# Kernel tuning notes

Measured on AMD Instinct MI355X. Metric: run time of the kernel, lower is better.

Reference implementation:

```python
import jax, jax.numpy as jnp
import numpy as np


def setup_inputs() -> dict:
    key = jax.random.key(0)
    k1, k2, k3 = jax.random.split(key, 3)
    B, T, D = 64, 256, 512
    real = jax.random.normal(k1, (B, T, D), dtype=jnp.float32)
    imag = jax.random.normal(k2, (B, T, D), dtype=jnp.float32)
    weight = jax.random.uniform(k3, (B, T, 1), dtype=jnp.float32)
    return {"real": real, "imag": imag, "weight": weight}


def reference(real, imag, weight):
    # Weighted complex outer-product mixture:
    #   out_r[b] = sum_t w[b,t] * (r_t r_t^T + i_t i_t^T)
    #   out_i[b] = sum_t w[b,t] * (i_t r_t^T - r_t i_t^T)
    # Equivalent to the original per-sample loop + TxDxD outer products,
    # but fused: scale one operand by w and contract over t directly.
    w = weight[..., 0]  # [B, T]
    rw = real * w[..., None]  # [B, T, D]
    iw = imag * w[..., None]
    out_r = jnp.einsum('btd,bte->bde', rw, real) + jnp.einsum('btd,bte->bde', iw, imag)
    out_i = jnp.einsum('btd,bte->bde', iw, real) - jnp.einsum('btd,bte->bde', rw, imag)
    return (out_r, out_i)
```

## Files before the change

kernel.cpp:

```cpp
#include <hip/hip_runtime.h>
#include <cstdint>
#include <cstddef>

#define BB 64
#define TT 256
#define DD 512
#define BK 32
#define TILEM 128

typedef short bf16x8 __attribute__((ext_vector_type(8)));
typedef float f32x4  __attribute__((ext_vector_type(4)));
typedef int   i32x4  __attribute__((ext_vector_type(4)));

static __device__ __forceinline__ unsigned short f2bf(float x) {
  unsigned u = __builtin_bit_cast(unsigned, x) + 0x8000u;
  return (unsigned short)(u >> 16);
}

__global__ __launch_bounds__(256, 2)
void ComplexMixture_54838142435828_kernel(const float* __restrict__ re,
                                          const float* __restrict__ im,
                                          const float* __restrict__ wt,
                                          float* __restrict__ out) {
  __shared__ __attribute__((aligned(16))) unsigned short sAr[4 * 128 * 8];
  __shared__ __attribute__((aligned(16))) unsigned short sAi[4 * 128 * 8];
  __shared__ __attribute__((aligned(16))) unsigned short sBr[4 * 128 * 8];
  __shared__ __attribute__((aligned(16))) unsigned short sBi[4 * 128 * 8];
  __shared__ float sw[TT];

  const int tid = threadIdx.x;

  const int L = blockIdx.x;
  const int c = L & 7;
  const int s = L >> 3;
  const int b  = c * 8 + (s >> 4);
  const int t5 = s & 15;
  const int d0 = (t5 >> 2) * TILEM;
  const int e0 = (t5 & 3) * TILEM;

  sw[tid] = wt[b * TT + tid];

  const int lane = tid & 63;
  const int wid  = tid >> 6;
  const int wm = (wid >> 1) * 64;
  const int wn = (wid & 1) * 64;
  const int quad = lane >> 4;
  const int l16  = lane & 15;

  f32x4 accR[4][4], accI[4][4];
  #pragma unroll
  for (int mt = 0; mt < 4; ++mt)
    #pragma unroll
    for (int nt = 0; nt < 4; ++nt) {
      accR[mt][nt] = (f32x4){0.f, 0.f, 0.f, 0.f};
      accI[mt][nt] = (f32x4){0.f, 0.f, 0.f, 0.f};
    }

  const int sd = tid & 127;
  const int kh = tid >> 7;

  for (int kt = 0; kt < TT; kt += BK) {
    __syncthreads();

    const int kb = kt + kh * 16;
    const size_t rowBase = ((size_t)(b * TT + kb)) * DD;

    {
      const float* pr = re + rowBase + d0 + sd;
      const float* pi = im + rowBase + d0 + sd;
      #pragma unroll
      for (int cc = 0; cc < 2; ++cc) {
        union { unsigned short h[8]; i32x4 q; } ur, ui;
        #pragma unroll
        for (int j = 0; j < 8; ++j) {
          const int k = cc * 8 + j;
          const float wv = sw[kb + k];
          ur.h[j] = f2bf(pr[(size_t)k * DD] * wv);
          ui.h[j] = f2bf(pi[(size_t)k * DD] * wv);
        }
        const int off = ((kh * 2 + cc) * 128 + sd) * 8;
        *(i32x4*)&sAr[off] = ur.q;
        *(i32x4*)&sAi[off] = ui.q;
      }
    }
    {
      const float* qr = re + rowBase + e0 + sd;
      const float* qi = im + rowBase + e0 + sd;
      #pragma unroll
      for (int cc = 0; cc < 2; ++cc) {
        union { unsigned short h[8]; i32x4 q; } ur, ui;
        #pragma unroll
        for (int j = 0; j < 8; ++j) {
          const int k = cc * 8 + j;
          ur.h[j] = f2bf(qr[(size_t)k * DD]);
          ui.h[j] = f2bf(qi[(size_t)k * DD]);
        }
        const int off = ((kh * 2 + cc) * 128 + sd) * 8;
        *(i32x4*)&sBr[off] = ur.q;
        *(i32x4*)&sBi[off] = ui.q;
      }
    }
    __syncthreads();

    bf16x8 aR[4], aI[4], bR[4], bI[4];
    #pragma unroll
    for (int t = 0; t < 4; ++t) {
      const int offA = (quad * 128 + wm + t * 16 + l16) * 8;
      const int offB = (quad * 128 + wn + t * 16 + l16) * 8;
      aR[t] = *(const bf16x8*)&sAr[offA];
      aI[t] = *(const bf16x8*)&sAi[offA];
      bR[t] = *(const bf16x8*)&sBr[offB];
      bI[t] = *(const bf16x8*)&sBi[offB];
    }
    #pragma unroll
    for (int mt = 0; mt < 4; ++mt) {
      const bf16x8 aRn = aR[mt] ^ (bf16x8)((short)0x8000);
      #pragma unroll
      for (int nt = 0; nt < 4; ++nt) {
        accR[mt][nt] = __builtin_amdgcn_mfma_f32_16x16x32_bf16(aR[mt], bR[nt], accR[mt][nt], 0, 0, 0);
        accR[mt][nt] = __builtin_amdgcn_mfma_f32_16x16x32_bf16(aI[mt], bI[nt], accR[mt][nt], 0, 0, 0);
        accI[mt][nt] = __builtin_amdgcn_mfma_f32_16x16x32_bf16(aI[mt], bR[nt], accI[mt][nt], 0, 0, 0);
        accI[mt][nt] = __builtin_amdgcn_mfma_f32_16x16x32_bf16(aRn,    bI[nt], accI[mt][nt], 0, 0, 0);
      }
    }
  }

  const size_t NOFF = (size_t)BB * DD * DD;
  #pragma unroll
  for (int mt = 0; mt < 4; ++mt) {
    #pragma unroll
    for (int r = 0; r < 4; ++r) {
      const int drow = d0 + wm + mt * 16 + quad * 4 + r;
      const size_t rowOff = ((size_t)(b * DD + drow)) * DD;
      #pragma unroll
      for (int nt = 0; nt < 4; ++nt) {
        const int ecol = e0 + wn + nt * 16 + l16;
        out[rowOff + ecol]        = accR[mt][nt][r];
        out[NOFF + rowOff + ecol] = accI[mt][nt][r];
      }
    }
  }
}

extern "C" void kernel_launch(void* const* d_in, const int* in_sizes, int n_in,
                              void* d_out, int out_size, void* d_ws, size_t ws_size,
                              hipStream_t stream) {
  const float* re = (const float*)d_in[0];
  const float* im = (const float*)d_in[1];
  const float* wt = (const float*)d_in[2];
  float* out = (float*)d_out;
  ComplexMixture_54838142435828_kernel<<<dim3(1024), dim3(256), 0, stream>>>(re, im, wt, out);
}
```

Measured before the change: 216.0 us.

## Stage raw fp32 tiles via global_load_lds and convert to bf16 at fragment load

Replaces the per-thread strided scalar global loads plus bf16 conversion into shared memory with direct global-to-LDS 16-byte DMA loads of raw fp32 rows. Weighting and bf16 conversion move to the fragment-read stage, where each wave reads fp32 from LDS and packs its own operands. This is meant to cut global load instruction count and VGPR pressure during staging. In exchange, LDS footprint doubles (64KB fp32), occupancy may drop, and each wave repeats the conversion work with scalar LDS reads that can hit bank conflicts.

```diff
diff --git a/kernel.cpp b/kernel.cpp
--- a/kernel.cpp
+++ b/kernel.cpp
@@ -10,7 +10,9 @@
 
 typedef short bf16x8 __attribute__((ext_vector_type(8)));
 typedef float f32x4  __attribute__((ext_vector_type(4)));
-typedef int   i32x4  __attribute__((ext_vector_type(4)));
+
+typedef __attribute__((address_space(1))) const void* gptr_t;
+typedef __attribute__((address_space(3))) void* sptr_t;
 
 static __device__ __forceinline__ unsigned short f2bf(float x) {
   unsigned u = __builtin_bit_cast(unsigned, x) + 0x8000u;
@@ -22,10 +24,7 @@
                                           const float* __restrict__ im,
                                           const float* __restrict__ wt,
                                           float* __restrict__ out) {
-  __shared__ __attribute__((aligned(16))) unsigned short sAr[4 * 128 * 8];
-  __shared__ __attribute__((aligned(16))) unsigned short sAi[4 * 128 * 8];
-  __shared__ __attribute__((aligned(16))) unsigned short sBr[4 * 128 * 8];
-  __shared__ __attribute__((aligned(16))) unsigned short sBi[4 * 128 * 8];
+  __shared__ __attribute__((aligned(16))) float sT[4 * BK * 128];
   __shared__ float sw[TT];
 
   const int tid = threadIdx.x;
@@ -47,6 +46,11 @@
   const int quad = lane >> 4;
   const int l16  = lane & 15;
 
+  const int scol = (wid & 2) ? e0 : d0;
+  const float* sbase = (wid & 1) ? im : re;
+  const int ksub  = lane >> 5;
+  const int dloc4 = (lane & 31) * 4;
+
   f32x4 accR[4][4], accI[4][4];
   #pragma unroll
   for (int mt = 0; mt < 4; ++mt)
@@ -56,71 +60,57 @@
       accI[mt][nt] = (f32x4){0.f, 0.f, 0.f, 0.f};
     }
 
-  const int sd = tid & 127;
-  const int kh = tid >> 7;
-
   for (int kt = 0; kt < TT; kt += BK) {
     __syncthreads();
 
-    const int kb = kt + kh * 16;
-    const size_t rowBase = ((size_t)(b * TT + kb)) * DD;
-
-    {
-      const float* pr = re + rowBase + d0 + sd;
-      const float* pi = im + rowBase + d0 + sd;
-      #pragma unroll
-      for (int cc = 0; cc < 2; ++cc) {
-        union { unsigned short h[8]; i32x4 q; } ur, ui;
-        #pragma unroll
-        for (int j = 0; j < 8; ++j) {
-          const int k = cc * 8 + j;
-          const float wv = sw[kb + k];
-          ur.h[j] = f2bf(pr[(size_t)k * DD] * wv);
-          ui.h[j] = f2bf(pi[(size_t)k * DD] * wv);
-        }
-        const int off = ((kh * 2 + cc) * 128 + sd) * 8;
-        *(i32x4*)&sAr[off] = ur.q;
-        *(i32x4*)&sAi[off] = ui.q;
-      }
-    }
-    {
-      const float* qr = re + rowBase + e0 + sd;
-      const float* qi = im + rowBase + e0 + sd;
-      #pragma unroll
-      for (int cc = 0; cc < 2; ++cc) {
-        union { unsigned short h[8]; i32x4 q; } ur, ui;
-        #pragma unroll
-        for (int j = 0; j < 8; ++j) {
-          const int k = cc * 8 + j;
-          ur.h[j] = f2bf(qr[(size_t)k * DD]);
-          ui.h[j] = f2bf(qi[(size_t)k * DD]);
-        }
-        const int off = ((kh * 2 + cc) * 128 + sd) * 8;
-        *(i32x4*)&sBr[off] = ur.q;
-        *(i32x4*)&sBi[off] = ui.q;
-      }
+    const float* gsrc = sbase + ((size_t)(b * TT + kt + ksub)) * DD + scol + dloc4;
+    float* lbase = &sT[wid * (BK * 128)];
+    #pragma unroll
+    for (int p = 0; p < 16; ++p) {
+      __builtin_amdgcn_global_load_lds((gptr_t)(const void*)(gsrc + (size_t)(2 * p) * DD),
+                                       (sptr_t)(void*)(lbase + p * 256),
+                                       16, 0, 0);
     }
     __syncthreads();
 
-    bf16x8 aR[4], aI[4], bR[4], bI[4];
+    float wv[8];
     #pragma unroll
-    for (int t = 0; t < 4; ++t) {
-      const int offA = (quad * 128 + wm + t * 16 + l16) * 8;
-      const int offB = (quad * 128 + wn + t * 16 + l16) * 8;
-      aR[t] = *(const bf16x8*)&sAr[offA];
-      aI[t] = *(const bf16x8*)&sAi[offA];
-      bR[t] = *(const bf16x8*)&sBr[offB];
-      bI[t] = *(const bf16x8*)&sBi[offB];
+    for (int j = 0; j < 8; ++j) wv[j] = sw[kt + quad * 8 + j];
+
+    bf16x8 bR[4], bI[4];
+    #pragma unroll
+    for (int nt = 0; nt < 4; ++nt) {
+      const int dl = wn + nt * 16 + l16;
+      union { unsigned short h[8]; bf16x8 v; } ur, ui;
+      #pragma unroll
+      for (int j = 0; j < 8; ++j) {
+        ur.h[j] = f2bf(sT[2 * (BK * 128) + (quad * 8 + j) * 128 + dl]);
+        ui.h[j] = f2bf(sT[3 * (BK * 128) + (quad * 8 + j) * 128 + dl]);
+      }
+      bR[nt] = ur.v;
+      bI[nt] = ui.v;
     }
+
     #pragma unroll
     for (int mt = 0; mt < 4; ++mt) {
-      const bf16x8 aRn = aR[mt] ^ (bf16x8)((short)0x8000);
+      const int dl = wm + mt * 16 + l16;
+      union { unsigned short h[8]; bf16x8 v; } ur, ui;
+      #pragma unroll
+      for (int j = 0; j < 8; ++j) {
+        const float r = sT[0 * (BK * 128) + (quad * 8 + j) * 128 + dl] * wv[j];
+        const float i = sT[1 * (BK * 128) + (quad * 8 + j) * 128 + dl] * wv[j];
+        ur.h[j] = f2bf(r);
+        ui.h[j] = f2bf(i);
+      }
+      const bf16x8 aR = ur.v;
+      const bf16x8 aI = ui.v;
+      const bf16x8 aRn = aR ^ (bf16x8)((short)0x8000);
       #pragma unroll
       for (int nt = 0; nt < 4; ++nt) {
-        accR[mt][nt] = __builtin_amdgcn_mfma_f32_16x16x32_bf16(aR[mt], bR[nt], accR[mt][nt], 0, 0, 0);
-        accR[mt][nt] = __builtin_amdgcn_mfma_f32_16x16x32_bf16(aI[mt], bI[nt], accR[mt][nt], 0, 0, 0);
-        accI[mt][nt] = __builtin_amdgcn_mfma_f32_16x16x32_bf16(aI[mt], bR[nt], accI[mt][nt], 0, 0, 0);
-        accI[mt][nt] = __builtin_amdgcn_mfma_f32_16x16x32_bf16(aRn,    bI[nt], accI[mt][nt], 0, 0, 0);
+        accR[mt][nt] = __builtin_amdgcn_mfma_f32_16x16x32_bf16(aR,  bR[nt], accR[mt][nt], 0, 0, 0);
+        accR[mt][nt] = __builtin_amdgcn_mfma_f32_16x16x32_bf16(aI,  bI[nt], accR[mt][nt], 0, 0, 0);
+        accI[mt][nt] = __builtin_amdgcn_mfma_f32_16x16x32_bf16(aI,  bR[nt], accI[mt][nt], 0, 0, 0);
+        accI[mt][nt] = __builtin_amdgcn_mfma_f32_16x16x32_bf16(aRn, bI[nt], accI[mt][nt], 0, 0, 0);
       }
     }
   }
```

Result: slower. 225.8 us (+4.5%).
